# Kernel optimization log

Hardware: AMD Instinct MI355X
Metric: run time of the kernel (lower is better)

Reference implementation:

```python
import jax, jax.numpy as jnp
import numpy as np

N = 100000
E = 3200000
IN_DIM = 128
OUT_DIM = 128
BN_EPS = 1e-5
LEAKY_SLOPE = 0.01


def setup_inputs() -> dict:
    key = jax.random.key(0)
    ks = jax.random.split(key, 6)
    fea = jax.random.normal(ks[0], (N, IN_DIM), dtype=jnp.float32)
    edges = jax.random.randint(ks[1], (2, E), 0, N, dtype=jnp.int64)
    Wlin = jax.random.normal(ks[2], (IN_DIM, IN_DIM), dtype=jnp.float32) * (1.0 / np.sqrt(IN_DIM))
    blin = jax.random.normal(ks[3], (IN_DIM,), dtype=jnp.float32) * 0.01
    gamma = jnp.ones((IN_DIM,), dtype=jnp.float32)
    beta = jnp.zeros((IN_DIM,), dtype=jnp.float32)
    Wg = jax.random.normal(ks[4], (OUT_DIM, IN_DIM), dtype=jnp.float32) * (1.0 / np.sqrt(IN_DIM))
    bg = jnp.zeros((OUT_DIM,), dtype=jnp.float32)
    return {"fea": fea, "edges": edges, "Wlin": Wlin, "blin": blin,
            "gamma": gamma, "beta": beta, "Wg": Wg, "bg": bg}


def reference(fea, edges, Wlin, blin, gamma, beta, Wg, bg):
    n = fea.shape[0]
    # Linear (in_dim -> in_dim)
    x = fea @ Wlin.T + blin
    # BatchNorm1d, training-mode batch statistics over the node dimension
    mean = jnp.mean(x, axis=0)
    var = jnp.var(x, axis=0)
    x = gamma * (x - mean) * jax.lax.rsqrt(var + BN_EPS) + beta
    # Dropout(p=0.0) is identity; LeakyReLU
    x = jnp.where(x >= 0, x, LEAKY_SLOPE * x)
    # GCNConv: h = x W^T, then D^-1/2 (A+I) D^-1/2 aggregation + bias
    h = x @ Wg.T  # [N, out_dim]
    self_idx = jnp.arange(n, dtype=edges.dtype)
    src = jnp.concatenate([edges[0], self_idx])
    dst = jnp.concatenate([edges[1], self_idx])
    deg = jax.ops.segment_sum(jnp.ones_like(dst, dtype=h.dtype), dst, num_segments=n)
    dinv = jnp.where(deg > 0, jax.lax.rsqrt(deg), 0.0)
    norm = dinv[src] * dinv[dst]  # [E+N]
    msgs = norm[:, None] * h[src]  # [E+N, out_dim]
    out = jax.ops.segment_sum(msgs, dst, num_segments=n) + bg
    # LogSoftmax over feature dim
    return jax.nn.log_softmax(out, axis=1)
```

## Files before the change

kernel.cpp:

```cpp
#include <hip/hip_runtime.h>
#include <math.h>

#define LEAKY 0.01f
#define BN_EPS 1e-5f
#define NBLK 512
#define EBUF 10240

typedef unsigned int uint;
typedef float f32x2 __attribute__((ext_vector_type(2)));
typedef float f32x4 __attribute__((ext_vector_type(4)));
typedef short bf16x8 __attribute__((ext_vector_type(8)));

__device__ __forceinline__ float bflo(uint v) { return __uint_as_float(v << 16); }
__device__ __forceinline__ float bfhi(uint v) { return __uint_as_float(v & 0xffff0000u); }
__device__ __forceinline__ uint packbf(float a, float b) {
    uint ua = __float_as_uint(a), ub = __float_as_uint(b);
    ua += 0x7fffu + ((ua >> 16) & 1u);
    ub += 0x7fffu + ((ub >> 16) & 1u);
    return (ua >> 16) | (ub & 0xffff0000u);
}

__device__ __forceinline__ int detect_i64(const int* __restrict__ raw) {
    int t = threadIdx.x & 63;
    unsigned long long b = __ballot(raw[2 * t + 1] != 0);
    return b == 0ull;
}

__device__ __forceinline__ void build_bbase(const int* __restrict__ btot,
                                            int NBUK, int* bb, int* sd)
{
    const int t = threadIdx.x;
    int a0 = (2 * t     < NBUK) ? btot[2 * t]     : 0;
    int a1 = (2 * t + 1 < NBUK) ? btot[2 * t + 1] : 0;
    int s = a0 + a1;
    sd[t] = s;
    __syncthreads();
    for (int o = 1; o < 256; o <<= 1) {
        int u = (t >= o) ? sd[t - o] : 0;
        __syncthreads();
        sd[t] += u;
        __syncthreads();
    }
    int ex = sd[t] - s;
    bb[2 * t]     = ex;
    bb[2 * t + 1] = ex + a0;
    __syncthreads();
}

__global__ __launch_bounds__(256) void k_prep(const float* __restrict__ Wlin,
                                              const float* __restrict__ Wg,
                                              uint* __restrict__ Wlinb,
                                              uint* __restrict__ Wgb,
                                              float* __restrict__ sums)
{
    const int idx = blockIdx.x * 256 + threadIdx.x;
    if (blockIdx.x == 0) sums[threadIdx.x] = 0.f;
    if (idx < 8192) {
        Wlinb[idx] = packbf(Wlin[2 * idx], Wlin[2 * idx + 1]);
    } else {
        int j = idx - 8192;
        Wgb[j] = packbf(Wg[2 * j], Wg[2 * j + 1]);
    }
}

__global__ __launch_bounds__(256) void k_bhist(const void* __restrict__ edges, int E,
                                               int* __restrict__ histm, int NBUK)
{
    __shared__ int hh[512];
    for (int b = threadIdx.x; b < 512; b += 256) hh[b] = 0;
    const int isI64 = detect_i64((const int*)edges);
    __syncthreads();

    const long long* e64 = (const long long*)edges;
    const int*       e32 = (const int*)edges;
    const int chunk = (E + NBLK - 1) / NBLK;
    const int lo = blockIdx.x * chunk;
    const int hi = min(lo + chunk, E);
    for (int e = lo + threadIdx.x; e < hi; e += 256) {
        int dst = isI64 ? (int)e64[(size_t)E + e] : e32[(size_t)E + e];
        atomicAdd(&hh[dst >> 8], 1);
    }
    __syncthreads();
    for (int b = threadIdx.x; b < NBUK; b += 256)
        histm[(size_t)b * NBLK + blockIdx.x] = hh[b];
}

__global__ __launch_bounds__(512) void k_bscan(int* __restrict__ histm,
                                               int* __restrict__ btot)
{
    __shared__ int sd[512];
    const int bkt = blockIdx.x;
    const int t = threadIdx.x;
    int v = histm[(size_t)bkt * NBLK + t];
    sd[t] = v;
    __syncthreads();
    for (int o = 1; o < 512; o <<= 1) {
        int u = (t >= o) ? sd[t - o] : 0;
        __syncthreads();
        sd[t] += u;
        __syncthreads();
    }
    histm[(size_t)bkt * NBLK + t] = sd[t] - v;
    if (t == 511) btot[bkt] = sd[511];
}

__global__ __launch_bounds__(256) void k_binscatter(const void* __restrict__ edges, int E,
                                                    const int* __restrict__ histm,
                                                    const int* __restrict__ btot,
                                                    uint* __restrict__ bins, int NBUK)
{
    __shared__ int cur[512];
    __shared__ int bb[512];
    __shared__ int sd[256];
    const int isI64 = detect_i64((const int*)edges);
    build_bbase(btot, NBUK, bb, sd);
    for (int b = threadIdx.x; b < NBUK; b += 256)
        cur[b] = bb[b] + histm[(size_t)b * NBLK + blockIdx.x];
    __syncthreads();

    const long long* e64 = (const long long*)edges;
    const int*       e32 = (const int*)edges;
    const int chunk = (E + NBLK - 1) / NBLK;
    const int lo = blockIdx.x * chunk;
    const int hi = min(lo + chunk, E);
    for (int e = lo + threadIdx.x; e < hi; e += 256) {
        int src, dst;
        if (isI64) { src = (int)e64[e]; dst = (int)e64[(size_t)E + e]; }
        else       { src = e32[e];      dst = e32[(size_t)E + e]; }
        int pos = atomicAdd(&cur[dst >> 8], 1);
        bins[pos] = (uint)src | ((uint)(dst & 255) << 24);
    }
}

__global__ __launch_bounds__(256) void k_csrdeg(const uint* __restrict__ bins,
                                                const int* __restrict__ btot,
                                                int* __restrict__ cnt,
                                                float* __restrict__ dinv,
                                                int* __restrict__ offs,
                                                uint* __restrict__ csr,
                                                int N, int NBUK)
{
    __shared__ uint ebuf[EBUF];
    __shared__ int bb[512];
    __shared__ int sd[256];
    __shared__ int c[256];
    const int bkt = blockIdx.x;
    const int t = threadIdx.x;
    build_bbase(btot, NBUK, bb, sd);
    const int lo    = bb[bkt];
    const int total = btot[bkt];
    c[t] = 0;
    __syncthreads();

    const bool fits = (total <= EBUF);
    for (int i = t; i < total; i += 256) {
        uint e = bins[lo + i];
        if (fits) ebuf[i] = e;
        atomicAdd(&c[e >> 24], 1);
    }
    __syncthreads();

    const int node = (bkt << 8) + t;
    const int deg  = c[t];
    if (node < N) {
        cnt[node]  = deg;
        dinv[node] = rsqrtf((float)(deg + 1));
    }
    sd[t] = deg;
    __syncthreads();
    for (int o = 1; o < 256; o <<= 1) {
        int u = (t >= o) ? sd[t - o] : 0;
        __syncthreads();
        sd[t] += u;
        __syncthreads();
    }
    const int off = lo + sd[t] - deg;
    if (node < N) offs[node] = off;
    c[t] = off;
    __syncthreads();
    for (int i = t; i < total; i += 256) {
        uint e = fits ? ebuf[i] : bins[lo + i];
        int pos = atomicAdd(&c[e >> 24], 1);
        csr[pos] = e & 0x00ffffffu;
    }
}

__global__ __launch_bounds__(256) void k_lin(const float* __restrict__ fea,
                                             const uint* __restrict__ Wb,
                                             const float* __restrict__ bias,
                                             uint* __restrict__ xb,
                                             float* __restrict__ sums, int N)
{
    __shared__ uint xls[64][68];
    __shared__ float sred[16][128];
    __shared__ float qred[16][128];
    const int tid  = threadIdx.x;
    const int r0   = blockIdx.x * 64;
    const int lane = tid & 63;
    const int w    = tid >> 6;
    const int fr   = lane & 15;
    const int fk   = lane >> 4;

    #pragma unroll
    for (int it = 0; it < 8; ++it) {
        int flat = it * 256 + tid;
        int row  = flat >> 5;
        int c4   = flat & 31;
        int r    = r0 + row;
        float4 v = make_float4(0.f, 0.f, 0.f, 0.f);
        if (r < N) v = *reinterpret_cast<const float4*>(&fea[(size_t)r * 128 + c4 * 4]);
        xls[row][c4 * 2]     = packbf(v.x, v.y);
        xls[row][c4 * 2 + 1] = packbf(v.z, v.w);
    }
    __syncthreads();

    bf16x8 a[4];
    #pragma unroll
    for (int kk = 0; kk < 4; ++kk)
        a[kk] = *reinterpret_cast<const bf16x8*>(&xls[w * 16 + fr][kk * 16 + fk * 4]);

    f32x4 acc[8] = {};
    #pragma unroll
    for (int jt = 0; jt < 8; ++jt) {
        #pragma unroll
        for (int kk = 0; kk < 4; ++kk) {
            bf16x8 b = *reinterpret_cast<const bf16x8*>(
                &Wb[(size_t)(jt * 16 + fr) * 64 + kk * 16 + fk * 4]);
            acc[jt] = __builtin_amdgcn_mfma_f32_16x16x32_bf16(a[kk], b, acc[jt], 0, 0, 0);
        }
    }
    __syncthreads();

    #pragma unroll
    for (int jt = 0; jt < 8; ++jt) {
        float bj = bias[jt * 16 + fr];
        float sl = 0.f, ql = 0.f;
        #pragma unroll
        for (int r = 0; r < 4; ++r) {
            int gr = r0 + w * 16 + fk * 4 + r;
            float val = acc[jt][r] + bj;
            val = (gr < N) ? val : 0.f;
            acc[jt][r] = val;
            sl += val; ql += val * val;
        }
        sred[w * 4 + fk][jt * 16 + fr] = sl;
        qred[w * 4 + fk][jt * 16 + fr] = ql;
    }
    __syncthreads();
    if (tid < 128) {
        float S = 0.f, Q = 0.f;
        #pragma unroll
        for (int g = 0; g < 16; ++g) { S += sred[g][tid]; Q += qred[g][tid]; }
        atomicAdd(&sums[tid], S);
        atomicAdd(&sums[128 + tid], Q);
    }
    #pragma unroll
    for (int jt = 0; jt < 8; ++jt) {
        #pragma unroll
        for (int r = 0; r < 4; ++r) {
            float val = acc[jt][r];
            float pv  = __shfl_xor(val, 1);
            if ((lane & 1) == 0) {
                int gr = r0 + w * 16 + fk * 4 + r;
                if (gr < N)
                    xb[(size_t)gr * 64 + jt * 8 + (fr >> 1)] = packbf(val, pv);
            }
        }
    }
}

__global__ __launch_bounds__(256) void k_h(const uint* __restrict__ xb,
                                           const uint* __restrict__ Wb,
                                           const float* __restrict__ sums,
                                           const float* __restrict__ gamma,
                                           const float* __restrict__ beta,
                                           const float* __restrict__ dinv,
                                           float invN,
                                           uint* __restrict__ hb, int N)
{
    __shared__ uint xls[64][68];
    __shared__ float aff[256];
    const int tid  = threadIdx.x;
    const int r0   = blockIdx.x * 64;
    const int lane = tid & 63;
    const int w    = tid >> 6;
    const int fr   = lane & 15;
    const int fk   = lane >> 4;

    if (tid < 128) {
        float mean = sums[tid] * invN;
        float var  = sums[128 + tid] * invN - mean * mean;
        float coef = gamma[tid] * rsqrtf(var + BN_EPS);
        aff[tid]       = coef;
        aff[128 + tid] = beta[tid] - coef * mean;
    }
    __syncthreads();

    #pragma unroll
    for (int it = 0; it < 16; ++it) {
        int flat = it * 256 + tid;
        int row  = flat >> 6;
        int u    = flat & 63;
        int r    = r0 + row;
        uint v   = (r < N) ? xb[(size_t)r * 64 + u] : 0u;
        float y0 = fmaf(aff[2 * u],     bflo(v), aff[128 + 2 * u]);
        float y1 = fmaf(aff[2 * u + 1], bfhi(v), aff[128 + 2 * u + 1]);
        y0 = (y0 >= 0.f) ? y0 : LEAKY * y0;
        y1 = (y1 >= 0.f) ? y1 : LEAKY * y1;
        xls[row][u] = packbf(y0, y1);
    }
    __syncthreads();

    bf16x8 a[4];
    #pragma unroll
    for (int kk = 0; kk < 4; ++kk)
        a[kk] = *reinterpret_cast<const bf16x8*>(&xls[w * 16 + fr][kk * 16 + fk * 4]);

    f32x4 acc[8] = {};
    #pragma unroll
    for (int jt = 0; jt < 8; ++jt) {
        #pragma unroll
        for (int kk = 0; kk < 4; ++kk) {
            bf16x8 b = *reinterpret_cast<const bf16x8*>(
                &Wb[(size_t)(jt * 16 + fr) * 64 + kk * 16 + fk * 4]);
            acc[jt] = __builtin_amdgcn_mfma_f32_16x16x32_bf16(a[kk], b, acc[jt], 0, 0, 0);
        }
    }

    float dv[4];
    #pragma unroll
    for (int r = 0; r < 4; ++r) {
        int gr = r0 + w * 16 + fk * 4 + r;
        dv[r] = (gr < N) ? dinv[gr] : 0.f;
    }

    #pragma unroll
    for (int jt = 0; jt < 8; ++jt) {
        #pragma unroll
        for (int r = 0; r < 4; ++r) {
            float val = acc[jt][r] * dv[r];
            float p1  = __shfl_xor(val, 1);
            uint lo16 = (uint)__builtin_amdgcn_cvt_pk_fp8_f32(val, p1, 0, false) & 0xffffu;
            uint hi16 = __shfl_xor(lo16, 2);
            if ((fr & 3) == 0) {
                int gr = r0 + w * 16 + fk * 4 + r;
                if (gr < N)
                    hb[(size_t)gr * 32 + jt * 4 + (fr >> 2)] = lo16 | (hi16 << 16);
            }
        }
    }
}

__global__ __launch_bounds__(256) void k_agg(const uint* __restrict__ hb,
                                             const uint* __restrict__ csr,
                                             const int* __restrict__ offs,
                                             const int* __restrict__ cnt,
                                             const float* __restrict__ dinv,
                                             const float* __restrict__ bg,
                                             float* __restrict__ out, int N)
{
    const int wid  = (blockIdx.x * blockDim.x + threadIdx.x) >> 6;
    const int lane = threadIdx.x & 63;
    if (wid >= N) return;
    const int i = wid;
    const int p = lane & 15;
    const int q = lane >> 4;

    f32x2 acc[4] = {};
    const int start = offs[i];
    const int m     = cnt[i];

    for (int base = 0; base < m; base += 64) {
        const int nb = min(64, m - base);
        uint sx = 0;
        if (lane < nb)
            sx = __builtin_nontemporal_load(&csr[start + base + lane]);
        for (int j = 0; j < nb; j += 8) {
            #pragma unroll
            for (int hh = 0; hh < 2; ++hh) {
                int eidx = j + hh * 4 + q;
                int   s  = __shfl((int)sx, eidx);
                float msk = (eidx < nb) ? 1.f : 0.f;
                const uint2 v = *reinterpret_cast<const uint2*>(
                    &hb[(size_t)(uint)s * 32 + p * 2]);
                f32x2 f01 = __builtin_amdgcn_cvt_pk_f32_fp8((int)v.x, false);
                f32x2 f23 = __builtin_amdgcn_cvt_pk_f32_fp8((int)v.x, true);
                f32x2 f45 = __builtin_amdgcn_cvt_pk_f32_fp8((int)v.y, false);
                f32x2 f67 = __builtin_amdgcn_cvt_pk_f32_fp8((int)v.y, true);
                acc[0] += f01 * msk;
                acc[1] += f23 * msk;
                acc[2] += f45 * msk;
                acc[3] += f67 * msk;
            }
        }
    }

    #pragma unroll
    for (int r = 0; r < 4; ++r) {
        acc[r].x += __shfl_xor(acc[r].x, 16);
        acc[r].y += __shfl_xor(acc[r].y, 16);
        acc[r].x += __shfl_xor(acc[r].x, 32);
        acc[r].y += __shfl_xor(acc[r].y, 32);
    }

    const uint2 sv = *reinterpret_cast<const uint2*>(&hb[(size_t)i * 32 + p * 2]);
    f32x2 s01 = __builtin_amdgcn_cvt_pk_f32_fp8((int)sv.x, false);
    f32x2 s23 = __builtin_amdgcn_cvt_pk_f32_fp8((int)sv.x, true);
    f32x2 s45 = __builtin_amdgcn_cvt_pk_f32_fp8((int)sv.y, false);
    f32x2 s67 = __builtin_amdgcn_cvt_pk_f32_fp8((int)sv.y, true);
    acc[0] += s01; acc[1] += s23; acc[2] += s45; acc[3] += s67;

    const float d0 = dinv[i];
    float4 b0 = *reinterpret_cast<const float4*>(&bg[p * 8]);
    float4 b1 = *reinterpret_cast<const float4*>(&bg[p * 8 + 4]);
    float v0 = fmaf(d0, acc[0].x, b0.x);
    float v1 = fmaf(d0, acc[0].y, b0.y);
    float v2 = fmaf(d0, acc[1].x, b0.z);
    float v3 = fmaf(d0, acc[1].y, b0.w);
    float v4 = fmaf(d0, acc[2].x, b1.x);
    float v5 = fmaf(d0, acc[2].y, b1.y);
    float v6 = fmaf(d0, acc[3].x, b1.z);
    float v7 = fmaf(d0, acc[3].y, b1.w);

    float mx = fmaxf(fmaxf(fmaxf(v0, v1), fmaxf(v2, v3)),
                     fmaxf(fmaxf(v4, v5), fmaxf(v6, v7)));
    #pragma unroll
    for (int o = 8; o > 0; o >>= 1) mx = fmaxf(mx, __shfl_xor(mx, o));
    float sum = __expf(v0 - mx) + __expf(v1 - mx) + __expf(v2 - mx) + __expf(v3 - mx)
              + __expf(v4 - mx) + __expf(v5 - mx) + __expf(v6 - mx) + __expf(v7 - mx);
    #pragma unroll
    for (int o = 8; o > 0; o >>= 1) sum += __shfl_xor(sum, o);
    float ls = mx + __logf(sum);

    if (q == 0) {
        f32x4 o0 = {v0 - ls, v1 - ls, v2 - ls, v3 - ls};
        f32x4 o1 = {v4 - ls, v5 - ls, v6 - ls, v7 - ls};
        __builtin_nontemporal_store(o0, reinterpret_cast<f32x4*>(&out[(size_t)i * 128 + p * 8]));
        __builtin_nontemporal_store(o1, reinterpret_cast<f32x4*>(&out[(size_t)i * 128 + p * 8 + 4]));
    }
}

extern "C" void kernel_launch(void* const* d_in, const int* in_sizes, int n_in,
                              void* d_out, int out_size, void* d_ws, size_t ws_size,
                              hipStream_t stream)
{
    (void)n_in; (void)out_size; (void)ws_size;
    const float* fea   = (const float*)d_in[0];
    const void*  edges = d_in[1];
    const float* Wlin  = (const float*)d_in[2];
    const float* blin  = (const float*)d_in[3];
    const float* gamma = (const float*)d_in[4];
    const float* beta  = (const float*)d_in[5];
    const float* Wg    = (const float*)d_in[6];
    const float* bg    = (const float*)d_in[7];
    float* out = (float*)d_out;

    const int N    = in_sizes[0] / 128;
    const int E    = in_sizes[1] / 2;
    const int NBUK = (N + 255) >> 8;

    char* p = (char*)d_ws;
    size_t u0 = (size_t)N * 64 * 4;
    size_t u1 = (size_t)E * 4;
    uint*  xb   = (uint*)p;
    uint*  bins = (uint*)p;    p += (u0 > u1 ? u0 : u1);
    uint*  hb   = (uint*)p;    p += (size_t)N * 32 * 4;
    uint*  csr  = (uint*)p;    p += (size_t)E * 4;
    int*   histm = (int*)p;    p += (size_t)NBUK * NBLK * 4;
    float* sums = (float*)p;   p += 256 * 4;
    int*   cnt  = (int*)p;     p += (size_t)N * 4;
    int*   offs = (int*)p;     p += (size_t)N * 4;
    float* dinv = (float*)p;   p += (size_t)N * 4;
    int*   btot = (int*)p;     p += 512 * 4;
    uint*  Wlinb = (uint*)p;   p += 8192 * 4;
    uint*  Wgb   = (uint*)p;   p += 8192 * 4;

    k_prep<<<64, 256, 0, stream>>>(Wlin, Wg, Wlinb, Wgb, sums);

    k_bhist<<<NBLK, 256, 0, stream>>>(edges, E, histm, NBUK);
    k_bscan<<<NBUK, 512, 0, stream>>>(histm, btot);
    k_binscatter<<<NBLK, 256, 0, stream>>>(edges, E, histm, btot, bins, NBUK);
    k_csrdeg<<<NBUK, 256, 0, stream>>>(bins, btot, cnt, dinv, offs, csr, N, NBUK);

    k_lin<<<(N + 63) / 64, 256, 0, stream>>>(fea, Wlinb, blin, xb, sums, N);
    k_h<<<(N + 63) / 64, 256, 0, stream>>>(xb, Wgb, sums, gamma, beta, dinv,
                                           1.0f / (float)N, hb, N);

    k_agg<<<(N + 3) / 4, 256, 0, stream>>>(hb, csr, offs, cnt, dinv, bg, out, N);
}
```

Baseline: 250.1 us.

## Fuse linear layer with edge histogram and pad CSR rows with sentinel node

Merges the bucket-histogram kernel and the first linear/BN-stats kernel into one launch whose blocks split by role, so the compute-bound GEMM overlaps with the memory-bound edge scan. Each node's CSR row is padded to a multiple of eight with a sentinel index pointing at an extra zero row of hb. This lets the aggregation loop drop per-edge masking and multiplies. The cost is extra workspace (bins no longer aliased with xb), a larger CSR, and one more row of hb that k_h must write.

```diff
diff --git a/kernel.cpp b/kernel.cpp
--- a/kernel.cpp
+++ b/kernel.cpp
@@ -63,26 +63,117 @@
     }
 }
 
-__global__ __launch_bounds__(256) void k_bhist(const void* __restrict__ edges, int E,
-                                               int* __restrict__ histm, int NBUK)
-{
-    __shared__ int hh[512];
-    for (int b = threadIdx.x; b < 512; b += 256) hh[b] = 0;
-    const int isI64 = detect_i64((const int*)edges);
-    __syncthreads();
-
-    const long long* e64 = (const long long*)edges;
-    const int*       e32 = (const int*)edges;
-    const int chunk = (E + NBLK - 1) / NBLK;
-    const int lo = blockIdx.x * chunk;
-    const int hi = min(lo + chunk, E);
-    for (int e = lo + threadIdx.x; e < hi; e += 256) {
-        int dst = isI64 ? (int)e64[(size_t)E + e] : e32[(size_t)E + e];
-        atomicAdd(&hh[dst >> 8], 1);
-    }
-    __syncthreads();
-    for (int b = threadIdx.x; b < NBUK; b += 256)
-        histm[(size_t)b * NBLK + blockIdx.x] = hh[b];
+__global__ __launch_bounds__(256) void k_front(const float* __restrict__ fea,
+                                               const uint* __restrict__ Wb,
+                                               const float* __restrict__ bias,
+                                               uint* __restrict__ xb,
+                                               float* __restrict__ sums,
+                                               const void* __restrict__ edges, int E,
+                                               int* __restrict__ histm,
+                                               int NBUK, int N, int G_lin)
+{
+    __shared__ uint smem[4352];
+    const int tid = threadIdx.x;
+
+    if ((int)blockIdx.x >= G_lin) {
+        const int bid = blockIdx.x - G_lin;
+        int* hh = (int*)smem;
+        for (int b = tid; b < 512; b += 256) hh[b] = 0;
+        const int isI64 = detect_i64((const int*)edges);
+        __syncthreads();
+        const long long* e64 = (const long long*)edges;
+        const int*       e32 = (const int*)edges;
+        const int chunk = (E + NBLK - 1) / NBLK;
+        const int lo = bid * chunk;
+        const int hi = min(lo + chunk, E);
+        for (int e = lo + tid; e < hi; e += 256) {
+            int dst = isI64 ? (int)e64[(size_t)E + e] : e32[(size_t)E + e];
+            atomicAdd(&hh[dst >> 8], 1);
+        }
+        __syncthreads();
+        for (int b = tid; b < NBUK; b += 256)
+            histm[(size_t)b * NBLK + bid] = hh[b];
+        return;
+    }
+
+    const int r0   = blockIdx.x * 64;
+    const int lane = tid & 63;
+    const int w    = tid >> 6;
+    const int fr   = lane & 15;
+    const int fk   = lane >> 4;
+
+    #pragma unroll
+    for (int it = 0; it < 8; ++it) {
+        int flat = it * 256 + tid;
+        int row  = flat >> 5;
+        int c4   = flat & 31;
+        int r    = r0 + row;
+        float4 v = make_float4(0.f, 0.f, 0.f, 0.f);
+        if (r < N) v = *reinterpret_cast<const float4*>(&fea[(size_t)r * 128 + c4 * 4]);
+        smem[row * 68 + c4 * 2]     = packbf(v.x, v.y);
+        smem[row * 68 + c4 * 2 + 1] = packbf(v.z, v.w);
+    }
+    __syncthreads();
+
+    bf16x8 a[4];
+    #pragma unroll
+    for (int kk = 0; kk < 4; ++kk)
+        a[kk] = *reinterpret_cast<const bf16x8*>(
+            &smem[(w * 16 + fr) * 68 + kk * 16 + fk * 4]);
+
+    f32x4 acc[8] = {};
+    #pragma unroll
+    for (int jt = 0; jt < 8; ++jt) {
+        #pragma unroll
+        for (int kk = 0; kk < 4; ++kk) {
+            bf16x8 b = *reinterpret_cast<const bf16x8*>(
+                &Wb[(size_t)(jt * 16 + fr) * 64 + kk * 16 + fk * 4]);
+            acc[jt] = __builtin_amdgcn_mfma_f32_16x16x32_bf16(a[kk], b, acc[jt], 0, 0, 0);
+        }
+    }
+    __syncthreads();
+
+    float* sred = (float*)smem;
+    float* qred = sred + 2048;
+    #pragma unroll
+    for (int jt = 0; jt < 8; ++jt) {
+        float bj = bias[jt * 16 + fr];
+        float sl = 0.f, ql = 0.f;
+        #pragma unroll
+        for (int r = 0; r < 4; ++r) {
+            int gr = r0 + w * 16 + fk * 4 + r;
+            float val = acc[jt][r] + bj;
+            val = (gr < N) ? val : 0.f;
+            acc[jt][r] = val;
+            sl += val; ql += val * val;
+        }
+        sred[(w * 4 + fk) * 128 + jt * 16 + fr] = sl;
+        qred[(w * 4 + fk) * 128 + jt * 16 + fr] = ql;
+    }
+    __syncthreads();
+    if (tid < 128) {
+        float S = 0.f, Q = 0.f;
+        #pragma unroll
+        for (int g = 0; g < 16; ++g) {
+            S += sred[g * 128 + tid];
+            Q += qred[g * 128 + tid];
+        }
+        atomicAdd(&sums[tid], S);
+        atomicAdd(&sums[128 + tid], Q);
+    }
+    #pragma unroll
+    for (int jt = 0; jt < 8; ++jt) {
+        #pragma unroll
+        for (int r = 0; r < 4; ++r) {
+            float val = acc[jt][r];
+            float pv  = __shfl_xor(val, 1);
+            if ((lane & 1) == 0) {
+                int gr = r0 + w * 16 + fk * 4 + r;
+                if (gr < N)
+                    xb[(size_t)gr * 64 + jt * 8 + (fr >> 1)] = packbf(val, pv);
+            }
+        }
+    }
 }
 
 __global__ __launch_bounds__(512) void k_bscan(int* __restrict__ histm,
@@ -134,7 +225,7 @@
 
 __global__ __launch_bounds__(256) void k_csrdeg(const uint* __restrict__ bins,
                                                 const int* __restrict__ btot,
-                                                int* __restrict__ cnt,
+                                                int* __restrict__ pcnt,
                                                 float* __restrict__ dinv,
                                                 int* __restrict__ offs,
                                                 uint* __restrict__ csr,
@@ -162,11 +253,12 @@
 
     const int node = (bkt << 8) + t;
     const int deg  = c[t];
+    const int pdeg = (deg + 7) & ~7;
     if (node < N) {
-        cnt[node]  = deg;
+        pcnt[node] = pdeg;
         dinv[node] = rsqrtf((float)(deg + 1));
     }
-    sd[t] = deg;
+    sd[t] = pdeg;
     __syncthreads();
     for (int o = 1; o < 256; o <<= 1) {
         int u = (t >= o) ? sd[t - o] : 0;
@@ -174,99 +266,17 @@
         sd[t] += u;
         __syncthreads();
     }
-    const int off = lo + sd[t] - deg;
-    if (node < N) offs[node] = off;
-    c[t] = off;
+    const int myoff = lo + (bkt << 11) + sd[t] - pdeg;
+    if (node < N) offs[node] = myoff;
+    c[t] = myoff;
     __syncthreads();
     for (int i = t; i < total; i += 256) {
         uint e = fits ? ebuf[i] : bins[lo + i];
         int pos = atomicAdd(&c[e >> 24], 1);
         csr[pos] = e & 0x00ffffffu;
     }
-}
-
-__global__ __launch_bounds__(256) void k_lin(const float* __restrict__ fea,
-                                             const uint* __restrict__ Wb,
-                                             const float* __restrict__ bias,
-                                             uint* __restrict__ xb,
-                                             float* __restrict__ sums, int N)
-{
-    __shared__ uint xls[64][68];
-    __shared__ float sred[16][128];
-    __shared__ float qred[16][128];
-    const int tid  = threadIdx.x;
-    const int r0   = blockIdx.x * 64;
-    const int lane = tid & 63;
-    const int w    = tid >> 6;
-    const int fr   = lane & 15;
-    const int fk   = lane >> 4;
-
-    #pragma unroll
-    for (int it = 0; it < 8; ++it) {
-        int flat = it * 256 + tid;
-        int row  = flat >> 5;
-        int c4   = flat & 31;
-        int r    = r0 + row;
-        float4 v = make_float4(0.f, 0.f, 0.f, 0.f);
-        if (r < N) v = *reinterpret_cast<const float4*>(&fea[(size_t)r * 128 + c4 * 4]);
-        xls[row][c4 * 2]     = packbf(v.x, v.y);
-        xls[row][c4 * 2 + 1] = packbf(v.z, v.w);
-    }
-    __syncthreads();
-
-    bf16x8 a[4];
-    #pragma unroll
-    for (int kk = 0; kk < 4; ++kk)
-        a[kk] = *reinterpret_cast<const bf16x8*>(&xls[w * 16 + fr][kk * 16 + fk * 4]);
-
-    f32x4 acc[8] = {};
-    #pragma unroll
-    for (int jt = 0; jt < 8; ++jt) {
-        #pragma unroll
-        for (int kk = 0; kk < 4; ++kk) {
-            bf16x8 b = *reinterpret_cast<const bf16x8*>(
-                &Wb[(size_t)(jt * 16 + fr) * 64 + kk * 16 + fk * 4]);
-            acc[jt] = __builtin_amdgcn_mfma_f32_16x16x32_bf16(a[kk], b, acc[jt], 0, 0, 0);
-        }
-    }
-    __syncthreads();
-
-    #pragma unroll
-    for (int jt = 0; jt < 8; ++jt) {
-        float bj = bias[jt * 16 + fr];
-        float sl = 0.f, ql = 0.f;
-        #pragma unroll
-        for (int r = 0; r < 4; ++r) {
-            int gr = r0 + w * 16 + fk * 4 + r;
-            float val = acc[jt][r] + bj;
-            val = (gr < N) ? val : 0.f;
-            acc[jt][r] = val;
-            sl += val; ql += val * val;
-        }
-        sred[w * 4 + fk][jt * 16 + fr] = sl;
-        qred[w * 4 + fk][jt * 16 + fr] = ql;
-    }
-    __syncthreads();
-    if (tid < 128) {
-        float S = 0.f, Q = 0.f;
-        #pragma unroll
-        for (int g = 0; g < 16; ++g) { S += sred[g][tid]; Q += qred[g][tid]; }
-        atomicAdd(&sums[tid], S);
-        atomicAdd(&sums[128 + tid], Q);
-    }
-    #pragma unroll
-    for (int jt = 0; jt < 8; ++jt) {
-        #pragma unroll
-        for (int r = 0; r < 4; ++r) {
-            float val = acc[jt][r];
-            float pv  = __shfl_xor(val, 1);
-            if ((lane & 1) == 0) {
-                int gr = r0 + w * 16 + fk * 4 + r;
-                if (gr < N)
-                    xb[(size_t)gr * 64 + jt * 8 + (fr >> 1)] = packbf(val, pv);
-            }
-        }
-    }
+    for (int k2 = deg; k2 < pdeg; ++k2)
+        csr[myoff + k2] = (uint)N;
 }
 
 __global__ __launch_bounds__(256) void k_h(const uint* __restrict__ xb,
@@ -344,7 +354,7 @@
             uint hi16 = __shfl_xor(lo16, 2);
             if ((fr & 3) == 0) {
                 int gr = r0 + w * 16 + fk * 4 + r;
-                if (gr < N)
+                if (gr <= N)
                     hb[(size_t)gr * 32 + jt * 4 + (fr >> 2)] = lo16 | (hi16 << 16);
             }
         }
@@ -354,7 +364,7 @@
 __global__ __launch_bounds__(256) void k_agg(const uint* __restrict__ hb,
                                              const uint* __restrict__ csr,
                                              const int* __restrict__ offs,
-                                             const int* __restrict__ cnt,
+                                             const int* __restrict__ pcnt,
                                              const float* __restrict__ dinv,
                                              const float* __restrict__ bg,
                                              float* __restrict__ out, int N)
@@ -365,32 +375,26 @@
     const int i = wid;
     const int p = lane & 15;
     const int q = lane >> 4;
+    const uint2* hbp = reinterpret_cast<const uint2*>(hb) + p;
 
     f32x2 acc[4] = {};
     const int start = offs[i];
-    const int m     = cnt[i];
+    const int m     = pcnt[i];
 
     for (int base = 0; base < m; base += 64) {
         const int nb = min(64, m - base);
-        uint sx = 0;
+        uint sx = (uint)N;
         if (lane < nb)
             sx = __builtin_nontemporal_load(&csr[start + base + lane]);
         for (int j = 0; j < nb; j += 8) {
             #pragma unroll
             for (int hh = 0; hh < 2; ++hh) {
-                int eidx = j + hh * 4 + q;
-                int   s  = __shfl((int)sx, eidx);
-                float msk = (eidx < nb) ? 1.f : 0.f;
-                const uint2 v = *reinterpret_cast<const uint2*>(
-                    &hb[(size_t)(uint)s * 32 + p * 2]);
-                f32x2 f01 = __builtin_amdgcn_cvt_pk_f32_fp8((int)v.x, false);
-                f32x2 f23 = __builtin_amdgcn_cvt_pk_f32_fp8((int)v.x, true);
-                f32x2 f45 = __builtin_amdgcn_cvt_pk_f32_fp8((int)v.y, false);
-                f32x2 f67 = __builtin_amdgcn_cvt_pk_f32_fp8((int)v.y, true);
-                acc[0] += f01 * msk;
-                acc[1] += f23 * msk;
-                acc[2] += f45 * msk;
-                acc[3] += f67 * msk;
+                int s = __shfl((int)sx, j + hh * 4 + q);
+                const uint2 v = hbp[(uint)s * 16];
+                acc[0] += __builtin_amdgcn_cvt_pk_f32_fp8((int)v.x, false);
+                acc[1] += __builtin_amdgcn_cvt_pk_f32_fp8((int)v.x, true);
+                acc[2] += __builtin_amdgcn_cvt_pk_f32_fp8((int)v.y, false);
+                acc[3] += __builtin_amdgcn_cvt_pk_f32_fp8((int)v.y, true);
             }
         }
     }
@@ -403,12 +407,11 @@
         acc[r].y += __shfl_xor(acc[r].y, 32);
     }
 
-    const uint2 sv = *reinterpret_cast<const uint2*>(&hb[(size_t)i * 32 + p * 2]);
-    f32x2 s01 = __builtin_amdgcn_cvt_pk_f32_fp8((int)sv.x, false);
-    f32x2 s23 = __builtin_amdgcn_cvt_pk_f32_fp8((int)sv.x, true);
-    f32x2 s45 = __builtin_amdgcn_cvt_pk_f32_fp8((int)sv.y, false);
-    f32x2 s67 = __builtin_amdgcn_cvt_pk_f32_fp8((int)sv.y, true);
-    acc[0] += s01; acc[1] += s23; acc[2] += s45; acc[3] += s67;
+    const uint2 sv = hbp[(uint)i * 16];
+    acc[0] += __builtin_amdgcn_cvt_pk_f32_fp8((int)sv.x, false);
+    acc[1] += __builtin_amdgcn_cvt_pk_f32_fp8((int)sv.x, true);
+    acc[2] += __builtin_amdgcn_cvt_pk_f32_fp8((int)sv.y, false);
+    acc[3] += __builtin_amdgcn_cvt_pk_f32_fp8((int)sv.y, true);
 
     const float d0 = dinv[i];
     float4 b0 = *reinterpret_cast<const float4*>(&bg[p * 8]);
@@ -458,17 +461,16 @@
     const int N    = in_sizes[0] / 128;
     const int E    = in_sizes[1] / 2;
     const int NBUK = (N + 255) >> 8;
+    const int GLIN = (N + 63) / 64;
 
     char* p = (char*)d_ws;
-    size_t u0 = (size_t)N * 64 * 4;
-    size_t u1 = (size_t)E * 4;
-    uint*  xb   = (uint*)p;
-    uint*  bins = (uint*)p;    p += (u0 > u1 ? u0 : u1);
-    uint*  hb   = (uint*)p;    p += (size_t)N * 32 * 4;
-    uint*  csr  = (uint*)p;    p += (size_t)E * 4;
+    uint*  xb   = (uint*)p;    p += (size_t)N * 64 * 4;
+    uint*  bins = (uint*)p;    p += (size_t)E * 4;
+    uint*  hb   = (uint*)p;    p += ((size_t)N + 1) * 32 * 4;
+    uint*  csr  = (uint*)p;    p += ((size_t)E + ((size_t)NBUK << 11)) * 4;
     int*   histm = (int*)p;    p += (size_t)NBUK * NBLK * 4;
     float* sums = (float*)p;   p += 256 * 4;
-    int*   cnt  = (int*)p;     p += (size_t)N * 4;
+    int*   pcnt = (int*)p;     p += (size_t)N * 4;
     int*   offs = (int*)p;     p += (size_t)N * 4;
     float* dinv = (float*)p;   p += (size_t)N * 4;
     int*   btot = (int*)p;     p += 512 * 4;
@@ -477,14 +479,15 @@
 
     k_prep<<<64, 256, 0, stream>>>(Wlin, Wg, Wlinb, Wgb, sums);
 
-    k_bhist<<<NBLK, 256, 0, stream>>>(edges, E, histm, NBUK);
+    k_front<<<GLIN + NBLK, 256, 0, stream>>>(fea, Wlinb, blin, xb, sums,
+                                             edges, E, histm, NBUK, N, GLIN);
+
     k_bscan<<<NBUK, 512, 0, stream>>>(histm, btot);
     k_binscatter<<<NBLK, 256, 0, stream>>>(edges, E, histm, btot, bins, NBUK);
-    k_csrdeg<<<NBUK, 256, 0, stream>>>(bins, btot, cnt, dinv, offs, csr, N, NBUK);
-
-    k_lin<<<(N + 63) / 64, 256, 0, stream>>>(fea, Wlinb, blin, xb, sums, N);
-    k_h<<<(N + 63) / 64, 256, 0, stream>>>(xb, Wgb, sums, gamma, beta, dinv,
+    k_csrdeg<<<NBUK, 256, 0, stream>>>(bins, btot, pcnt, dinv, offs, csr, N, NBUK);
+
+    k_h<<<(N + 64) / 64, 256, 0, stream>>>(xb, Wgb, sums, gamma, beta, dinv,
                                            1.0f / (float)N, hb, N);
 
-    k_agg<<<(N + 3) / 4, 256, 0, stream>>>(hb, csr, offs, cnt, dinv, bg, out, N);
-}
+    k_agg<<<(N + 3) / 4, 256, 0, stream>>>(hb, csr, offs, pcnt, dinv, bg, out, N);
+}
```

After: 244.4 us. -2.3%, faster.
